# Kernel optimization log

Hardware: AMD Instinct MI355X
Metric: run time of the kernel (lower is better)

Reference implementation:

```python
import jax, jax.numpy as jnp
import numpy as np

B, T, S, D = 32, 1024, 1024, 512
VOCAB = 1000
INSERT_TOK = jnp.array([1, 2], dtype=jnp.int64)


def setup_inputs() -> dict:
    key = jax.random.key(0)
    k1, k2, k3, k4, k5 = jax.random.split(key, 5)
    input_var = jax.random.randint(k1, (B, T), 0, VOCAB, dtype=jnp.int64)
    output = jax.random.normal(k2, (B, T, D), jnp.float32)
    context = jax.random.normal(k3, (B, S, D), jnp.float32)
    # nn.Linear(2*dim, dim): weight [D, 2D], bias [D]
    W = jax.random.normal(k4, (D, 2 * D), jnp.float32) / np.sqrt(2 * D)
    b = jax.random.normal(k5, (D,), jnp.float32) * 0.01
    return {"input_var": input_var, "output": output, "context": context,
            "di": 0, "W": W, "b": b}


def _hard_align(input_var, src_len):
    """Replicates the python double-loop: sequential 'inserted' counter per batch.
    Returns (j, valid): j[b,i] = column of the 1.0 in attn row i (torch negative
    indices wrapped), valid[b,i] = whether row i gets any 1.0 at all."""
    bsz, tgt_len = input_var.shape
    flags = jnp.isin(input_var, INSERT_TOK)  # [B,T] is token an insert token

    def step(inserted, xi):
        i, flag = xi  # i: scalar position, flag: [B]
        cond = (src_len >= i - inserted)                    # gate, per batch
        ins2 = inserted + jnp.where(cond & flag, 1, 0)      # increment before write
        j = i - ins2 - 1
        j = jnp.where(j < 0, j + src_len, j)                # torch negative-index wrap
        return ins2, (j, cond)

    idxs = jnp.arange(1, tgt_len, dtype=jnp.int32)
    init = jnp.zeros((bsz,), jnp.int32)  # init_inserted()
    _, (j_rows, valid) = jax.lax.scan(step, init, (idxs, flags[:, 1:].T))
    j_rows = j_rows.T      # [B,T-1]
    valid = valid.T        # [B,T-1]
    # row 0: attn[b,0,0] = 1.0 always
    j_full = jnp.concatenate([jnp.zeros((bsz, 1), j_rows.dtype), j_rows], axis=1)
    valid_full = jnp.concatenate([jnp.ones((bsz, 1), bool), valid], axis=1)
    return j_full, valid_full


def reference(input_var, output, context, di, W, b):
    bsz, tgt_len, hid = output.shape
    src_len = context.shape[1]
    j, valid = _hard_align(input_var, src_len)              # [B,T], [B,T]
    vf = valid[:, :, None].astype(output.dtype)
    # hard one-hot attention matrix (as the module materializes it)
    attn = jax.nn.one_hot(j, src_len, dtype=output.dtype) * vf  # [B,T,S]
    # mix = bmm(attn, context) == masked gather of context rows
    mix = jnp.take_along_axis(context, j[:, :, None].astype(jnp.int32), axis=1) * vf
    combined = jnp.concatenate([mix, output], axis=-1)      # [B,T,2D]
    out = jnp.tanh(combined @ W.T + b)                      # [B,T,D]
    return out, attn
```

## Files before the change

kernel.cpp:

```cpp
#include <hip/hip_runtime.h>
#include <hip/hip_bf16.h>

#define B_ 32
#define T_ 1024
#define S_ 1024
#define D_ 512
#define M_ (B_*T_)
#define N_ D_
#define K_ (2*D_)

typedef __attribute__((ext_vector_type(8))) short bf16x8;
typedef __attribute__((ext_vector_type(4))) float f32x4;

__device__ inline unsigned short f2bf(float x) {
    union { float f; unsigned u; } v; v.f = x;
    unsigned r = v.u + 0x7FFFu + ((v.u >> 16) & 1u);
    return (unsigned short)(r >> 16);
}

__device__ inline unsigned cvt2bf(float lo, float hi) {
#if __has_builtin(__builtin_amdgcn_cvt_pk_bf16_f32)
    typedef __attribute__((ext_vector_type(2))) __bf16 bf2;
    union { bf2 v; unsigned u; } r;
    r.v = __builtin_amdgcn_cvt_pk_bf16_f32(lo, hi);
    return r.u;
#else
    return (unsigned)f2bf(lo) | ((unsigned)f2bf(hi) << 16);
#endif
}

__device__ inline float fast_tanh(float x) {
#if __has_builtin(__builtin_amdgcn_exp2f) && __has_builtin(__builtin_amdgcn_rcpf)
    const float e = __builtin_amdgcn_exp2f(x * 2.885390082f);
    const float r = __builtin_amdgcn_rcpf(e + 1.0f);
    return 1.0f - 2.0f * r;
#else
    return tanhf(x);
#endif
}

__global__ void align_kernel(const int* __restrict__ iv, int* __restrict__ jbuf) {
    const int b = blockIdx.x;
    const int lane = threadIdx.x;
    const int* row = iv + b * T_;
    int f[16];
    int local = 0;
    const int t0 = lane * 16;
    #pragma unroll
    for (int q = 0; q < 16; ++q) {
        const int t = t0 + q;
        const int tok = row[t];
        const int fl = (t > 0 && (tok == 1 || tok == 2)) ? 1 : 0;
        f[q] = fl;
        local += fl;
    }
    int incl = local;
    #pragma unroll
    for (int off = 1; off < 64; off <<= 1) {
        const int up = __shfl_up(incl, off, 64);
        if (lane >= off) incl += up;
    }
    int run = incl - local;
    #pragma unroll
    for (int q = 0; q < 16; ++q) {
        const int t = t0 + q;
        run += f[q];
        int j;
        if (t == 0) {
            j = 0;
        } else {
            j = t - run - 1;
            if (j < 0) j += S_;
        }
        jbuf[b * T_ + t] = j;
    }
}

__global__ void pack_w(const float* __restrict__ W, unsigned short* __restrict__ Wbf) {
    const int idx = blockIdx.x * blockDim.x + threadIdx.x;
    const f32x4 a = ((const f32x4*)W)[idx * 2];
    const f32x4 c = ((const f32x4*)W)[idx * 2 + 1];
    union { bf16x8 v; unsigned u[4]; } pk;
    pk.u[0] = cvt2bf(a[0], a[1]); pk.u[1] = cvt2bf(a[2], a[3]);
    pk.u[2] = cvt2bf(c[0], c[1]); pk.u[3] = cvt2bf(c[2], c[3]);
    *(bf16x8*)(Wbf + (size_t)idx * 8) = pk.v;
}

#define BM 128
#define BN 128
#define BK 64
#define NGEMM ((M_ / BM) * (N_ / BN))
#define NATTN 512

__global__ __launch_bounds__(256)
void gemm_attn(const unsigned short* __restrict__ Wbf,
               const float* __restrict__ bias,
               float* __restrict__ out,
               float* __restrict__ attn,
               const float* __restrict__ ctx,
               const float* __restrict__ outp,
               const int* __restrict__ jbuf) {
    const int bx = blockIdx.x;
    const int tid = threadIdx.x;

    if (bx >= NGEMM) {
        const int m0 = (bx - NGEMM) * 64;
        #pragma unroll 4
        for (int r = 0; r < 64; ++r) {
            const int row = m0 + r;
            const int j = jbuf[row];
            f32x4 v = {0.f, 0.f, 0.f, 0.f};
            if ((j >> 2) == tid) v[j & 3] = 1.0f;
            ((f32x4*)(attn + (size_t)row * S_))[tid] = v;
        }
        return;
    }

    __shared__ unsigned short As[BM * BK];
    __shared__ unsigned short Bs[BN * BK];

    const int lane = tid & 63;
    const int wave = tid >> 6;
    const int wm = wave >> 1, wn = wave & 1;
    const int l16 = lane & 15, quad = lane >> 4;

    const int bm = bx & 255;
    const int bn = bx >> 8;
    const int mBase = bm * BM;
    const int nBase = bn * BN;

    const int arow = tid >> 1;
    const int aseg = tid & 1;
    const int am   = mBase + arow;
    const int jm   = jbuf[am];
    const float* actx = ctx + ((size_t)((am >> 10) * S_ + jm)) * D_ + aseg * 32;
    const float* aoutp = outp + (size_t)am * D_ - D_ + aseg * 32;

    f32x4 acc[4][4] = {};

    for (int ko = 0; ko < K_; ko += BK) {
        {
            const float* srcA = (ko < D_) ? (actx + ko) : (aoutp + ko);
            f32x4 fa[8];
            #pragma unroll
            for (int i = 0; i < 8; ++i) fa[i] = ((const f32x4*)srcA)[i];
            #pragma unroll
            for (int c = 0; c < 4; ++c) {
                union { bf16x8 v; unsigned u[4]; } pk;
                pk.u[0] = cvt2bf(fa[c*2][0],   fa[c*2][1]);
                pk.u[1] = cvt2bf(fa[c*2][2],   fa[c*2][3]);
                pk.u[2] = cvt2bf(fa[c*2+1][0], fa[c*2+1][1]);
                pk.u[3] = cvt2bf(fa[c*2+1][2], fa[c*2+1][3]);
                const int q = aseg * 4 + c;
                *(bf16x8*)&As[(arow * 8 + (q ^ (arow & 7))) * 8] = pk.v;
            }
        }
        #pragma unroll
        for (int it = 0; it < 4; ++it) {
            const int chunk = it * 256 + tid;
            const int row = chunk >> 3;
            const int kc  = chunk & 7;
            const int gk8 = (kc ^ (row & 7)) * 8;
            const unsigned short* gB = Wbf + (size_t)(nBase + row) * K_ + ko + gk8;
            __builtin_amdgcn_global_load_lds(
                (const __attribute__((address_space(1))) void*)gB,
                (__attribute__((address_space(3))) void*)(Bs + chunk * 8), 16, 0, 0);
        }
        __syncthreads();

        #pragma unroll
        for (int ks = 0; ks < 2; ++ks) {
            bf16x8 af[4], bfr[4];
            #pragma unroll
            for (int mt = 0; mt < 4; ++mt) {
                const int r = wm * 64 + mt * 16 + l16;
                const int q = ks * 4 + quad;
                af[mt] = *(const bf16x8*)&As[(r * 8 + (q ^ (r & 7))) * 8];
            }
            #pragma unroll
            for (int nt = 0; nt < 4; ++nt) {
                const int r = wn * 64 + nt * 16 + l16;
                const int q = ks * 4 + quad;
                bfr[nt] = *(const bf16x8*)&Bs[(r * 8 + (q ^ (r & 7))) * 8];
            }
            #pragma unroll
            for (int mt = 0; mt < 4; ++mt)
                #pragma unroll
                for (int nt = 0; nt < 4; ++nt)
                    acc[mt][nt] = __builtin_amdgcn_mfma_f32_16x16x32_bf16(
                        af[mt], bfr[nt], acc[mt][nt], 0, 0, 0);
        }
        __syncthreads();
    }

    #pragma unroll
    for (int nt = 0; nt < 4; ++nt) {
        const int n = nBase + wn * 64 + nt * 16 + l16;
        const float bv = bias[n];
        #pragma unroll
        for (int mt = 0; mt < 4; ++mt) {
            #pragma unroll
            for (int r = 0; r < 4; ++r) {
                const int m = mBase + wm * 64 + mt * 16 + quad * 4 + r;
                out[(size_t)m * N_ + n] = fast_tanh(acc[mt][nt][r] + bv);
            }
        }
    }
}

extern "C" void kernel_launch(void* const* d_in, const int* in_sizes, int n_in,
                              void* d_out, int out_size, void* d_ws, size_t ws_size,
                              hipStream_t stream) {
    const int*   iv   = (const int*)d_in[0];
    const float* outp = (const float*)d_in[1];
    const float* ctx  = (const float*)d_in[2];
    const float* W    = (const float*)d_in[4];
    const float* bias = (const float*)d_in[5];

    float* out  = (float*)d_out;
    float* attn = out + (size_t)M_ * N_;

    int* jbuf = (int*)d_ws;
    unsigned short* Wbf = (unsigned short*)((char*)d_ws + (size_t)M_ * 4);

    align_kernel<<<B_, 64, 0, stream>>>(iv, jbuf);
    pack_w<<<(N_ * K_ / 8) / 256, 256, 0, stream>>>(W, Wbf);
    gemm_attn<<<NGEMM + NATTN, 256, 0, stream>>>(Wbf, bias, out, attn, ctx, outp, jbuf);
}
```

Baseline: 364.5 us.

## Coalesce A-tile loads, issue B loads before convert, schedule attn blocks first

Changes the A-tile fetch so each thread loads 8 consecutive floats from four rows (8 threads per row) instead of 32 floats from one row. Rows are now read across lanes in a coalesced pattern, and the B global_load_lds is issued before the bf16 conversion and LDS store so the two transfers overlap. The attention one-hot blocks are moved to the front of the grid, and launch_bounds now requests 4 blocks per SM. The cost is more pointer registers per thread and possible spills caused by the occupancy hint.

New measurement: 360.2 us. About the same (-1.2%).

```diff
diff --git a/kernel.cpp b/kernel.cpp
--- a/kernel.cpp
+++ b/kernel.cpp
@@ -92,7 +92,7 @@
 #define NGEMM ((M_ / BM) * (N_ / BN))
 #define NATTN 512
 
-__global__ __launch_bounds__(256)
+__global__ __launch_bounds__(256, 4)
 void gemm_attn(const unsigned short* __restrict__ Wbf,
                const float* __restrict__ bias,
                float* __restrict__ out,
@@ -103,8 +103,8 @@
     const int bx = blockIdx.x;
     const int tid = threadIdx.x;
 
-    if (bx >= NGEMM) {
-        const int m0 = (bx - NGEMM) * 64;
+    if (bx < NATTN) {
+        const int m0 = bx * 64;
         #pragma unroll 4
         for (int r = 0; r < 64; ++r) {
             const int row = m0 + r;
@@ -119,52 +119,60 @@
     __shared__ unsigned short As[BM * BK];
     __shared__ unsigned short Bs[BN * BK];
 
+    const int gbx  = bx - NATTN;
     const int lane = tid & 63;
     const int wave = tid >> 6;
     const int wm = wave >> 1, wn = wave & 1;
     const int l16 = lane & 15, quad = lane >> 4;
 
-    const int bm = bx & 255;
-    const int bn = bx >> 8;
+    const int bm = gbx & 255;
+    const int bn = gbx >> 8;
     const int mBase = bm * BM;
     const int nBase = bn * BN;
 
-    const int arow = tid >> 1;
-    const int aseg = tid & 1;
-    const int am   = mBase + arow;
-    const int jm   = jbuf[am];
-    const float* actx = ctx + ((size_t)((am >> 10) * S_ + jm)) * D_ + aseg * 32;
-    const float* aoutp = outp + (size_t)am * D_ - D_ + aseg * 32;
+    const int kc   = tid & 7;
+    const int rsub = tid >> 3;
+    const int sw   = kc ^ (rsub & 7);
+    const float* actx[4];
+    const float* aout[4];
+    #pragma unroll
+    for (int it = 0; it < 4; ++it) {
+        const int r = it * 32 + rsub;
+        const int m = mBase + r;
+        const int jm = jbuf[m];
+        actx[it] = ctx + ((size_t)((m >> 10) * S_ + jm)) * D_ + kc * 8;
+        aout[it] = outp + (size_t)m * D_ - D_ + kc * 8;
+    }
 
     f32x4 acc[4][4] = {};
 
     for (int ko = 0; ko < K_; ko += BK) {
-        {
-            const float* srcA = (ko < D_) ? (actx + ko) : (aoutp + ko);
-            f32x4 fa[8];
-            #pragma unroll
-            for (int i = 0; i < 8; ++i) fa[i] = ((const f32x4*)srcA)[i];
-            #pragma unroll
-            for (int c = 0; c < 4; ++c) {
-                union { bf16x8 v; unsigned u[4]; } pk;
-                pk.u[0] = cvt2bf(fa[c*2][0],   fa[c*2][1]);
-                pk.u[1] = cvt2bf(fa[c*2][2],   fa[c*2][3]);
-                pk.u[2] = cvt2bf(fa[c*2+1][0], fa[c*2+1][1]);
-                pk.u[3] = cvt2bf(fa[c*2+1][2], fa[c*2+1][3]);
-                const int q = aseg * 4 + c;
-                *(bf16x8*)&As[(arow * 8 + (q ^ (arow & 7))) * 8] = pk.v;
-            }
+        f32x4 fa[4][2];
+        #pragma unroll
+        for (int it = 0; it < 4; ++it) {
+            const float* src = (ko < D_) ? (actx[it] + ko) : (aout[it] + ko);
+            fa[it][0] = ((const f32x4*)src)[0];
+            fa[it][1] = ((const f32x4*)src)[1];
         }
         #pragma unroll
         for (int it = 0; it < 4; ++it) {
             const int chunk = it * 256 + tid;
             const int row = chunk >> 3;
-            const int kc  = chunk & 7;
-            const int gk8 = (kc ^ (row & 7)) * 8;
+            const int kcb = chunk & 7;
+            const int gk8 = (kcb ^ (row & 7)) * 8;
             const unsigned short* gB = Wbf + (size_t)(nBase + row) * K_ + ko + gk8;
             __builtin_amdgcn_global_load_lds(
                 (const __attribute__((address_space(1))) void*)gB,
                 (__attribute__((address_space(3))) void*)(Bs + chunk * 8), 16, 0, 0);
+        }
+        #pragma unroll
+        for (int it = 0; it < 4; ++it) {
+            union { bf16x8 v; unsigned u[4]; } pk;
+            pk.u[0] = cvt2bf(fa[it][0][0], fa[it][0][1]);
+            pk.u[1] = cvt2bf(fa[it][0][2], fa[it][0][3]);
+            pk.u[2] = cvt2bf(fa[it][1][0], fa[it][1][1]);
+            pk.u[3] = cvt2bf(fa[it][1][2], fa[it][1][3]);
+            *(bf16x8*)&As[(it * 256 + rsub * 8 + sw) * 8] = pk.v;
         }
         __syncthreads();
 
```
